# Performance work log

Hardware: AMD Instinct MI355X
Metric: run time of the kernel (lower is better)

## Reference

```python
import jax, jax.numpy as jnp
import numpy as np

TOKEN_SELF_ATTN_VALUE = -50000.0
EPS_NORM = 1e-12
EPS_SCATTER = 1e-5
COMMITMENT = 1e-4


def _l2norm(x):
    return x / jnp.maximum(jnp.linalg.norm(x, axis=-1, keepdims=True), EPS_NORM)


def _shift(x):
    # relative-position shift, faithful to the torch `shift` helper
    # x: [..., i, j] -> [..., i, j]
    *pre, i, j = x.shape
    x = jnp.concatenate([x, jnp.zeros((*pre, i, i), x.dtype)], axis=-1)  # [..., i, i+j]
    l = i + j - 1
    x = x.reshape(*pre, i * (i + j))
    pad = (-x.shape[-1]) % l
    x = jnp.concatenate([x, jnp.zeros((*pre, pad), x.dtype)], axis=-1)
    x = x.reshape(*pre, -1, l)
    return x[..., :i, i - 1:]


def setup_inputs() -> dict:
    key = jax.random.key(0)
    k1, k2, k3, k4 = jax.random.split(key, 4)
    b, h, t, d = 4, 8, 8192, 64
    c, wsz = 64, 128
    qk = jax.random.normal(k1, (b, h, t, d), jnp.float32)
    v = jax.random.normal(k2, (b, h, t, d), jnp.float32)
    means = jax.random.normal(k3, (h, c, d), jnp.float32)
    means = _l2norm(means)  # trained kmeans means are unit-normalized
    rel_w = jax.random.normal(k4, (wsz, h, d), jnp.float32) * 0.02
    return {"qk": qk, "v": v, "means": means, "rel_w": rel_w}


def reference(qk, v, means, rel_w):
    b, h, t, d = qk.shape
    c = means.shape[1]
    wsz = min(rel_w.shape[0], t)

    # ---- kmeans routing (eval path: no iterations, fixed means) ----
    k_routing = _l2norm(qk)                                   # [b,h,t,d]
    dists = jnp.einsum('bhld,hcd->bhlc', k_routing, means)    # cosine sims
    buckets = jnp.argmax(dists, axis=-1)                      # [b,h,t]
    # top-wsz tokens per cluster, sorted ascending (matches topk -> sort -> transpose)
    _, idx = jax.lax.top_k(jnp.swapaxes(dists, -1, -2), wsz)  # [b,h,c,wsz]
    indices = jnp.sort(idx, axis=-1).reshape(b, h, c * wsz)   # [b,h,c*wsz]

    # commitment loss against routed means (means is a non-trainable buffer)
    routed_means = means[jnp.arange(h)[None, :, None], buckets]  # [b,h,t,d]
    loss = jnp.mean((k_routing - routed_means) ** 2) * COMMITMENT

    # ---- gather routed windows ----
    qk_g = jnp.take_along_axis(qk, indices[..., None], axis=2).reshape(b, h, c, wsz, d)
    v_g = jnp.take_along_axis(v, indices[..., None], axis=2).reshape(b, h, c, wsz, d)
    q = qk_g
    k = _l2norm(qk_g)

    scale = d ** -0.5
    dots = jnp.einsum('bhnid,bhnjd->bhnij', q, k) * scale     # [b,h,c,wsz,wsz]
    rel = jnp.einsum('bhnid,jhd->bhnij', q, rel_w) * scale
    dots = dots + _shift(rel)

    # token cannot attend to itself within its window
    eye = jnp.eye(wsz, dtype=bool)
    dots = jnp.where(eye, TOKEN_SELF_ATTN_VALUE, dots)

    attn = jax.nn.softmax(dots, axis=-1)
    bo = jnp.einsum('bhnij,bhnjd->bhnid', attn, v_g).reshape(b, h, c * wsz, d)

    # ---- scatter-mean back to original token positions ----
    def scat(idx1, src1):  # idx1: [N], src1: [N,d]
        num = jnp.zeros((t, d), src1.dtype).at[idx1].add(src1)
        den = jnp.zeros((t, d), src1.dtype).at[idx1].add(jnp.ones_like(src1))
        return num / (den + EPS_SCATTER)

    out = jax.vmap(jax.vmap(scat))(indices, bo)               # [b,h,t,d]
    return out, loss
```

## Files before the change

kernel.cpp:

```cpp
#include <hip/hip_runtime.h>
#include <hip/hip_bf16.h>
#include <math.h>

#define NB 4
#define NH 8
#define TT 8192
#define DD 64
#define NC 64
#define WW 128
#define BHN 32
#define SCALE 0.125f
#define INVCAP 24
#define DTPB 64

typedef __bf16  bf16x8 __attribute__((ext_vector_type(8)));
typedef __bf16  bf16x4 __attribute__((ext_vector_type(4)));
typedef float   f32x4  __attribute__((ext_vector_type(4)));
typedef unsigned long long u64;
typedef unsigned int u32;

#define MFMA(a, b, c) __builtin_amdgcn_mfma_f32_16x16x32_bf16((a), (b), (c), 0, 0, 0)

__device__ __forceinline__ u32 fixkey32(float dv) {
    double k = ((double)dv + 1.0) * 2147483648.0;
    k = fmin(fmax(k, 0.0), 4294967295.0);
    return (u32)k;
}

#define QD_ADDR(row, gi) (((row) << 6) + ((((gi) ^ ((row) & 7))) << 3))

__global__ __launch_bounds__(256) void k_dists(
    const float* __restrict__ qk, const float* __restrict__ means,
    const float* __restrict__ rel_w, __bf16* __restrict__ relb,
    u32* __restrict__ keys, double* __restrict__ lossa)
{
    __shared__ __attribute__((aligned(16))) __bf16 qh[64 * 64], qm[64 * 64], ql[64 * 64];
    __shared__ __attribute__((aligned(16))) __bf16 ah[64 * 64], am[64 * 64], al[64 * 64];
    __shared__ float invS[DTPB], s2S[DTPB], mn2S[NC];
    __shared__ double red[4];

    const int bh = blockIdx.x, h = bh & 7, tid = threadIdx.x;
    const int t0 = blockIdx.y * DTPB;

    if (blockIdx.y == 0) {
        const float4* rw = (const float4*)rel_w;
#pragma unroll
        for (int k = 0; k < 2; k++) {
            const int i = bh * 512 + k * 256 + tid;
            const float4 v = rw[i];
            bf16x4 o;
            o[0] = (__bf16)v.x; o[1] = (__bf16)v.y; o[2] = (__bf16)v.z; o[3] = (__bf16)v.w;
            *(bf16x4*)(relb + i * 4) = o;
        }
    }

    {
        const int r = tid >> 2, qt = tid & 3;
        const float4* src = (const float4*)(means + (size_t)(h * NC + r) * DD + qt * 16);
        float4 f[4];
        f[0] = src[0]; f[1] = src[1]; f[2] = src[2]; f[3] = src[3];
        bf16x8 vh[2], vm[2], vl[2];
        float ssq = 0.f;
#pragma unroll
        for (int j = 0; j < 16; j++) {
            const float xx = ((const float*)f)[j];
            ssq = fmaf(xx, xx, ssq);
            const __bf16 hh_ = (__bf16)xx;
            const float r1 = xx - (float)hh_;
            const __bf16 mm_ = (__bf16)r1;
            const float r2 = r1 - (float)mm_;
            vh[j >> 3][j & 7] = hh_; vm[j >> 3][j & 7] = mm_; vl[j >> 3][j & 7] = (__bf16)r2;
        }
#pragma unroll
        for (int gg = 0; gg < 2; gg++) {
            const int dst = QD_ADDR(r, qt * 2 + gg);
            *(bf16x8*)(ah + dst) = vh[gg];
            *(bf16x8*)(am + dst) = vm[gg];
            *(bf16x8*)(al + dst) = vl[gg];
        }
        ssq += __shfl_xor(ssq, 1);
        ssq += __shfl_xor(ssq, 2);
        if (qt == 0) mn2S[r] = ssq;
    }
    {
        const int r = tid >> 2, qt = tid & 3;
        const float4* src = (const float4*)(qk + ((size_t)bh * TT + t0 + r) * DD + qt * 16);
        float4 f[4];
        f[0] = src[0]; f[1] = src[1]; f[2] = src[2]; f[3] = src[3];
        bf16x8 vh[2], vm[2], vl[2];
        float ssq = 0.f;
#pragma unroll
        for (int j = 0; j < 16; j++) {
            const float xx = ((const float*)f)[j];
            ssq = fmaf(xx, xx, ssq);
            const __bf16 hh_ = (__bf16)xx;
            const float r1 = xx - (float)hh_;
            const __bf16 mm_ = (__bf16)r1;
            const float r2 = r1 - (float)mm_;
            vh[j >> 3][j & 7] = hh_; vm[j >> 3][j & 7] = mm_; vl[j >> 3][j & 7] = (__bf16)r2;
        }
#pragma unroll
        for (int gg = 0; gg < 2; gg++) {
            const int dst = QD_ADDR(r, qt * 2 + gg);
            *(bf16x8*)(qh + dst) = vh[gg];
            *(bf16x8*)(qm + dst) = vm[gg];
            *(bf16x8*)(ql + dst) = vl[gg];
        }
        ssq += __shfl_xor(ssq, 1);
        ssq += __shfl_xor(ssq, 2);
        if (qt == 0) {
            const float inv = 1.0f / fmaxf(sqrtf(ssq), 1e-12f);
            invS[r] = inv;
            s2S[r] = ssq * inv * inv;
        }
    }
    __syncthreads();

    const int lane = tid & 63, wv = tid >> 6;
    const int lo = lane & 15, quad = lane >> 4;

    bf16x8 Bh[2], Bm[2], Bl[2];
    {
        const int row = wv * 16 + lo;
#pragma unroll
        for (int kh = 0; kh < 2; kh++) {
            const int src = QD_ADDR(row, kh * 4 + quad);
            Bh[kh] = *(const bf16x8*)(qh + src);
            Bm[kh] = *(const bf16x8*)(qm + src);
            Bl[kh] = *(const bf16x8*)(ql + src);
        }
    }

    f32x4 acc[4];
#pragma unroll
    for (int ct = 0; ct < 4; ct++) {
        bf16x8 Ah[2], Am[2], Al[2];
#pragma unroll
        for (int kh = 0; kh < 2; kh++) {
            const int src = QD_ADDR(ct * 16 + lo, kh * 4 + quad);
            Ah[kh] = *(const bf16x8*)(ah + src);
            Am[kh] = *(const bf16x8*)(am + src);
            Al[kh] = *(const bf16x8*)(al + src);
        }
        f32x4 a = (f32x4){0.f, 0.f, 0.f, 0.f};
        a = MFMA(Al[0], Bm[0], a); a = MFMA(Al[1], Bm[1], a);
        a = MFMA(Am[0], Bl[0], a); a = MFMA(Am[1], Bl[1], a);
        a = MFMA(Am[0], Bm[0], a); a = MFMA(Am[1], Bm[1], a);
        a = MFMA(Ah[0], Bl[0], a); a = MFMA(Ah[1], Bl[1], a);
        a = MFMA(Al[0], Bh[0], a); a = MFMA(Al[1], Bh[1], a);
        a = MFMA(Am[0], Bh[0], a); a = MFMA(Am[1], Bh[1], a);
        a = MFMA(Ah[0], Bm[0], a); a = MFMA(Ah[1], Bm[1], a);
        a = MFMA(Ah[0], Bh[0], a); a = MFMA(Ah[1], Bh[1], a);
        acc[ct] = a;
    }

    const int tok = wv * 16 + lo;
    const float inv = invS[tok];
    float rawmax = -3.0e38f; int cbest = 0;
    u32* kout = keys + (size_t)bh * NC * TT + (size_t)(t0 + tok);
#pragma unroll
    for (int ct = 0; ct < 4; ct++)
#pragma unroll
        for (int r = 0; r < 4; r++) {
            const float raw = acc[ct][r];
            const int c = ct * 16 + quad * 4 + r;
            if (raw > rawmax) { rawmax = raw; cbest = c; }
            kout[(size_t)c * TT] = fixkey32(raw * inv);
        }

#pragma unroll
    for (int off = 16; off < 64; off <<= 1) {
        const float ov = __shfl_xor(rawmax, off);
        const int   oc = __shfl_xor(cbest, off);
        if (ov > rawmax || (ov == rawmax && oc < cbest)) { rawmax = ov; cbest = oc; }
    }
    double lt_lane = 0.0;
    if (quad == 0)
        lt_lane = (double)(s2S[tok] + mn2S[cbest] - 2.0f * rawmax * inv);

#pragma unroll
    for (int o = 32; o; o >>= 1) lt_lane += __shfl_xor(lt_lane, o);
    if (lane == 0) red[wv] = lt_lane;
    __syncthreads();
    if (tid == 0) atomicAdd(lossa, red[0] + red[1] + red[2] + red[3]);
}

__global__ __launch_bounds__(256) void k_topk(
    const u32* __restrict__ keys, int* __restrict__ indices,
    unsigned int* __restrict__ cnt, unsigned short* __restrict__ inv)
{
    __shared__ unsigned int hist[4][256];
    __shared__ int wsum[8];
    __shared__ int bc_bin, bc_rank, bc_cnt;

    const int bhc = blockIdx.x, tid = threadIdx.x;
    const int wv = tid >> 6, lane = tid & 63;
    const int bh = bhc >> 6;

    u32 key[32];
    {
        const uint4* p = (const uint4*)(keys + (size_t)bhc * TT + tid * 32);
#pragma unroll
        for (int i = 0; i < 8; i++) {
            uint4 u = p[i];
            key[4*i] = u.x; key[4*i+1] = u.y; key[4*i+2] = u.z; key[4*i+3] = u.w;
        }
    }

    u32 thr = 0;
    int need = 128, gshift = 24, prevShift = 0;
    unsigned int* hb = &hist[0][0];

    for (int level = 0; level < 4; level++) {
        const int shift = 24 - 8 * level;
        hb[tid] = 0; hb[tid + 256] = 0; hb[tid + 512] = 0; hb[tid + 768] = 0;
        __syncthreads();
        unsigned int* hw = hist[wv];
        if (level == 0) {
#pragma unroll
            for (int i = 0; i < 32; i++)
                atomicAdd(&hw[key[i] >> 24], 1u);
        } else {
            const u32 pv = thr >> prevShift;
#pragma unroll
            for (int i = 0; i < 32; i++)
                if ((key[i] >> prevShift) == pv)
                    atomicAdd(&hw[(key[i] >> shift) & 255u], 1u);
        }
        __syncthreads();

        const int b = 255 - tid;
        const int c = hist[0][b] + hist[1][b] + hist[2][b] + hist[3][b];
        int incl = c;
#pragma unroll
        for (int o = 1; o < 64; o <<= 1) {
            const int v = __shfl_up(incl, o);
            if (lane >= o) incl += v;
        }
        if (lane == 63) wsum[wv] = incl;
        __syncthreads();
        int above = incl - c;
        for (int wj = 0; wj < wv; wj++) above += wsum[wj];
        if (above < need && above + c >= need) {
            bc_bin = b; bc_rank = above; bc_cnt = c;
        }
        __syncthreads();
        thr |= ((u32)bc_bin) << shift;
        need -= bc_rank;
        gshift = shift;
        prevShift = shift;
        if (bc_cnt == need || shift == 0) break;
    }

    const u32 tg = thr >> gshift;
    int cgt = 0, ceq = 0;
#pragma unroll
    for (int i = 0; i < 32; i++) {
        const u32 kg = key[i] >> gshift;
        cgt += (kg > tg) ? 1 : 0;
        ceq += (kg == tg) ? 1 : 0;
    }
    int ig = cgt, ie = ceq;
#pragma unroll
    for (int o = 1; o < 64; o <<= 1) {
        const int vg = __shfl_up(ig, o);
        const int ve = __shfl_up(ie, o);
        if (lane >= o) { ig += vg; ie += ve; }
    }
    if (lane == 63) { wsum[wv] = ig; wsum[4 + wv] = ie; }
    __syncthreads();
    int pgt = ig - cgt, peq = ie - ceq;
    for (int wj = 0; wj < wv; wj++) { pgt += wsum[wj]; peq += wsum[4 + wj]; }

    const int rneed = need;
    int* outp = indices + bhc * WW;
    unsigned int* cntb = cnt + (bh << 13);
    unsigned short* invb = inv + (((size_t)bh << 13) * INVCAP);
    const int cbase = (bhc & 63) * WW;
    int g = 0, e = 0;
#pragma unroll
    for (int i = 0; i < 32; i++) {
        const int tok = tid * 32 + i;
        const u32 kg = key[i] >> gshift;
        if (kg > tg) {
            const int tb = (peq + e < rneed) ? (peq + e) : rneed;
            const int wpos = pgt + g + tb;
            outp[wpos] = tok;
            const unsigned int pos = atomicAdd(&cntb[tok], 1u);
            if (pos < INVCAP) invb[(size_t)tok * INVCAP + pos] = (unsigned short)(cbase + wpos);
            g++;
        } else if (kg == tg) {
            if (peq + e < rneed) {
                const int wpos = pgt + g + peq + e;
                outp[wpos] = tok;
                const unsigned int pos = atomicAdd(&cntb[tok], 1u);
                if (pos < INVCAP) invb[(size_t)tok * INVCAP + pos] = (unsigned short)(cbase + wpos);
            }
            e++;
        }
    }
}

#define QS_ADDR(row, gi) (((row) << 6) + ((((gi) ^ ((row) & 7))) << 3))

__global__ __launch_bounds__(512) void k_attn(
    const float* __restrict__ qk, const float* __restrict__ vin,
    const __bf16* __restrict__ relb, const int* __restrict__ indices,
    float* __restrict__ bo)
{
    __shared__ __attribute__((aligned(16))) __bf16 uv[64 * 136];
    __shared__ __attribute__((aligned(16))) __bf16 rs[128 * 136];
    __shared__ float invs[128];

    const int tid  = threadIdx.x;
    const int lane = tid & 63;
    const int wv   = tid >> 6;
    const int lo   = lane & 15;
    const int quad = lane >> 4;
    const int rbase = wv * 16;

    const int bhc = blockIdx.x;
    const int bh  = bhc >> 6;
    const int h   = bh & 7;

    const int r  = tid >> 2;
    const int qp = tid & 3;
    const int rowidx = indices[bhc * WW + r];
    const size_t rowoff = ((size_t)bh * TT + rowidx) * DD + qp * 16;
    float4 q0, q1, q2, q3, vreg[4];
    {
        const float4* qsrc = (const float4*)(qk + rowoff);
        q0 = qsrc[0]; q1 = qsrc[1]; q2 = qsrc[2]; q3 = qsrc[3];
        const float4* vsrc = (const float4*)(vin + rowoff);
        vreg[0] = vsrc[0]; vreg[1] = vsrc[1]; vreg[2] = vsrc[2]; vreg[3] = vsrc[3];
    }
    {
        float ssq = q0.x*q0.x + q0.y*q0.y + q0.z*q0.z + q0.w*q0.w
                  + q1.x*q1.x + q1.y*q1.y + q1.z*q1.z + q1.w*q1.w
                  + q2.x*q2.x + q2.y*q2.y + q2.z*q2.z + q2.w*q2.w
                  + q3.x*q3.x + q3.y*q3.y + q3.z*q3.z + q3.w*q3.w;
        ssq += __shfl_xor(ssq, 1);
        ssq += __shfl_xor(ssq, 2);
        if (qp == 0) invs[r] = 1.0f / fmaxf(sqrtf(ssq), 1e-12f);
        bf16x8 va, vb;
        va[0]=(__bf16)q0.x; va[1]=(__bf16)q0.y; va[2]=(__bf16)q0.z; va[3]=(__bf16)q0.w;
        va[4]=(__bf16)q1.x; va[5]=(__bf16)q1.y; va[6]=(__bf16)q1.z; va[7]=(__bf16)q1.w;
        vb[0]=(__bf16)q2.x; vb[1]=(__bf16)q2.y; vb[2]=(__bf16)q2.z; vb[3]=(__bf16)q2.w;
        vb[4]=(__bf16)q3.x; vb[5]=(__bf16)q3.y; vb[6]=(__bf16)q3.z; vb[7]=(__bf16)q3.w;
        *(bf16x8*)(uv + QS_ADDR(r, qp * 2))     = va;
        *(bf16x8*)(uv + QS_ADDR(r, qp * 2 + 1)) = vb;
    }
    __syncthreads();

    f32x4 acc[8];

#pragma unroll
    for (int nt = 0; nt < 8; nt++) acc[nt] = (f32x4){0.f, 0.f, 0.f, 0.f};
#pragma unroll
    for (int k0 = 0; k0 < 64; k0 += 32) {
        bf16x8 qa = *(const bf16x8*)(uv + QS_ADDR(rbase + lo, (k0 >> 3) + quad));
#pragma unroll
        for (int nt = 0; nt < 8; nt++) {
            const bf16x8 wb = *(const bf16x8*)(relb + ((nt * 16 + lo) * 8 + h) * 64 + k0 + quad * 8);
            acc[nt] = MFMA(qa, wb, acc[nt]);
        }
    }
#pragma unroll
    for (int nt = 0; nt < 8; nt++)
#pragma unroll
        for (int rg = 0; rg < 4; rg++)
            rs[(rbase + quad * 4 + rg) * 136 + nt * 16 + lo] = (__bf16)acc[nt][rg];

#pragma unroll
    for (int nt = 0; nt < 8; nt++) acc[nt] = (f32x4){0.f, 0.f, 0.f, 0.f};
#pragma unroll
    for (int k0 = 0; k0 < 64; k0 += 32) {
        bf16x8 qa = *(const bf16x8*)(uv + QS_ADDR(rbase + lo, (k0 >> 3) + quad));
#pragma unroll
        for (int nt = 0; nt < 8; nt++) {
            bf16x8 qb = *(const bf16x8*)(uv + QS_ADDR(nt * 16 + lo, (k0 >> 3) + quad));
            acc[nt] = MFMA(qa, qb, acc[nt]);
        }
    }

    float inv_j[8];
#pragma unroll
    for (int nt = 0; nt < 8; nt++) inv_j[nt] = invs[nt * 16 + lo];

#pragma unroll
    for (int rg = 0; rg < 4; rg++) {
        const int i = rbase + quad * 4 + rg;
#pragma unroll
        for (int nt = 0; nt < 8; nt++) {
            const int j = nt * 16 + lo;
            float val = acc[nt][rg] * inv_j[nt] * SCALE;
            if (j <= i) val += SCALE * (float)rs[i * 136 + (j + 127 - i)];
            if (j == i) val = -50000.0f;
            acc[nt][rg] = val;
        }
    }

#pragma unroll
    for (int rg = 0; rg < 4; rg++) {
        float m = -3.0e38f;
#pragma unroll
        for (int nt = 0; nt < 8; nt++) m = fmaxf(m, acc[nt][rg]);
#pragma unroll
        for (int msk = 1; msk < 16; msk <<= 1) m = fmaxf(m, __shfl_xor(m, msk));
        float s = 0.f;
#pragma unroll
        for (int nt = 0; nt < 8; nt++) {
            const float e = __expf(acc[nt][rg] - m);
            acc[nt][rg] = e; s += e;
        }
#pragma unroll
        for (int msk = 1; msk < 16; msk <<= 1) s += __shfl_xor(s, msk);
        const float is = 1.0f / s;
        const int i = rbase + quad * 4 + rg;
#pragma unroll
        for (int nt = 0; nt < 8; nt++)
            rs[i * 136 + nt * 16 + lo] = (__bf16)(acc[nt][rg] * is);
    }
    __syncthreads();

    __bf16* vt = uv;
#pragma unroll
    for (int i = 0; i < 4; i++) {
        vt[(qp * 16 + 4*i + 0) * 136 + r] = (__bf16)vreg[i].x;
        vt[(qp * 16 + 4*i + 1) * 136 + r] = (__bf16)vreg[i].y;
        vt[(qp * 16 + 4*i + 2) * 136 + r] = (__bf16)vreg[i].z;
        vt[(qp * 16 + 4*i + 3) * 136 + r] = (__bf16)vreg[i].w;
    }
    __syncthreads();

    f32x4 accO[4];
#pragma unroll
    for (int nt = 0; nt < 4; nt++) accO[nt] = (f32x4){0.f, 0.f, 0.f, 0.f};
#pragma unroll
    for (int k0 = 0; k0 < 128; k0 += 32) {
        bf16x8 pa = *(const bf16x8*)(rs + (rbase + lo) * 136 + k0 + quad * 8);
#pragma unroll
        for (int nt = 0; nt < 4; nt++) {
            bf16x8 vb = *(const bf16x8*)(vt + (nt * 16 + lo) * 136 + k0 + quad * 8);
            accO[nt] = MFMA(pa, vb, accO[nt]);
        }
    }

    float* bb = bo + (size_t)bhc * (WW * DD);
#pragma unroll
    for (int rg = 0; rg < 4; rg++) {
        const int i = rbase + quad * 4 + rg;
#pragma unroll
        for (int nt = 0; nt < 4; nt++)
            bb[(size_t)i * DD + nt * 16 + lo] = accO[nt][rg];
    }
}

__global__ __launch_bounds__(256) void k_out(
    const float* __restrict__ bo, const unsigned int* __restrict__ cnt,
    const unsigned short* __restrict__ inv, const double* __restrict__ lossa,
    float* __restrict__ out)
{
    const int tid = threadIdx.x;
    const int g = blockIdx.x * 16 + (tid >> 4);
    const int l = tid & 15;
    const int bh = g >> 13;
    const unsigned int n = cnt[g];
    const int nc = (n < (unsigned)INVCAP) ? (int)n : INVCAP;
    const unsigned short* ip = inv + (size_t)g * INVCAP;
    const float* bbase = bo + (((size_t)bh << 13) * DD) + l * 4;

    const uint4 ipv = *(const uint4*)ip;
    const int s0 = ipv.x & 0xffff, s1 = ipv.x >> 16;
    const int s2 = ipv.y & 0xffff, s3 = ipv.y >> 16;
    const int s4 = ipv.z & 0xffff, s5 = ipv.z >> 16;
    const int s6 = ipv.w & 0xffff, s7 = ipv.w >> 16;

    float4 a0 = {0.f,0.f,0.f,0.f}, a1 = a0, a2 = a0, a3 = a0;
    float4 a4 = a0, a5 = a0, a6 = a0, a7 = a0;
    if (nc > 0) a0 = *(const float4*)(bbase + (size_t)s0 * DD);
    if (nc > 1) a1 = *(const float4*)(bbase + (size_t)s1 * DD);
    if (nc > 2) a2 = *(const float4*)(bbase + (size_t)s2 * DD);
    if (nc > 3) a3 = *(const float4*)(bbase + (size_t)s3 * DD);
    if (nc > 4) a4 = *(const float4*)(bbase + (size_t)s4 * DD);
    if (nc > 5) a5 = *(const float4*)(bbase + (size_t)s5 * DD);
    if (nc > 6) a6 = *(const float4*)(bbase + (size_t)s6 * DD);
    if (nc > 7) a7 = *(const float4*)(bbase + (size_t)s7 * DD);

    float4 s;
    s.x = ((a0.x + a1.x) + (a2.x + a3.x)) + ((a4.x + a5.x) + (a6.x + a7.x));
    s.y = ((a0.y + a1.y) + (a2.y + a3.y)) + ((a4.y + a5.y) + (a6.y + a7.y));
    s.z = ((a0.z + a1.z) + (a2.z + a3.z)) + ((a4.z + a5.z) + (a6.z + a7.z));
    s.w = ((a0.w + a1.w) + (a2.w + a3.w)) + ((a4.w + a5.w) + (a6.w + a7.w));

    for (int e = 8; e < nc; e++) {
        const int slot = ip[e];
        const float4 v4 = *(const float4*)(bbase + (size_t)slot * DD);
        s.x += v4.x; s.y += v4.y; s.z += v4.z; s.w += v4.w;
    }

    const float r = 1.0f / ((float)n + 1e-5f);
    s.x *= r; s.y *= r; s.z *= r; s.w *= r;
    *(float4*)(out + (size_t)g * DD + l * 4) = s;
    if (g == 0 && l == 0) out[16777216] = (float)(lossa[0] * (0.0001 / 16777216.0));
}

extern "C" void kernel_launch(void* const* d_in, const int* in_sizes, int n_in,
                              void* d_out, int out_size, void* d_ws, size_t ws_size,
                              hipStream_t stream) {
    (void)in_sizes; (void)n_in; (void)ws_size; (void)out_size;
    const float* qk    = (const float*)d_in[0];
    const float* v     = (const float*)d_in[1];
    const float* means = (const float*)d_in[2];
    const float* rel_w = (const float*)d_in[3];
    float* out = (float*)d_out;

    char* ws = (char*)d_ws;
    const size_t KEYS_B = (size_t)BHN * NC * TT * 4;
    const size_t IDX_B  = (size_t)BHN * NC * WW * 4;
    const size_t CNT_B  = (size_t)BHN * TT * 4;
    const size_t INV_B  = (size_t)BHN * TT * INVCAP * 2;
    u32*            keys  = (u32*)ws;
    float*          bo    = (float*)ws;
    int*            idx   = (int*)(ws + KEYS_B);
    unsigned int*   cnt   = (unsigned int*)(ws + KEYS_B + IDX_B);
    double*         lossa = (double*)(ws + KEYS_B + IDX_B + CNT_B);
    unsigned short* inv   = (unsigned short*)(ws + KEYS_B + IDX_B + CNT_B + 4096);
    __bf16*         relb  = (__bf16*)(ws + KEYS_B + IDX_B + CNT_B + 4096 + INV_B);

    hipMemsetAsync(ws + KEYS_B + IDX_B, 0, CNT_B + 4096, stream);

    k_dists<<<dim3(BHN, TT / DTPB), 256, 0, stream>>>(qk, means, rel_w, relb, keys, lossa);
    k_topk<<<BHN * NC, 256, 0, stream>>>(keys, idx, cnt, inv);
    k_attn<<<BHN * NC, 512, 0, stream>>>(qk, v, relb, idx, bo);
    k_out<<<BHN * TT / 16, 256, 0, stream>>>(bo, cnt, inv, lossa, out);
}
```

Measured before the change: 326.2 us.

## Process four clusters per attention block with register prefetch of next tile

Each k_attn block now loops over four consecutive clusters instead of one, and the grid shrinks to match. While the current tile computes, the gathered q and v rows for the next tile are loaded into registers, so global gather latency overlaps with the MFMA and softmax work. The cost is fewer blocks (512 instead of 2048), which reduces parallelism across CUs. It also adds an extra barrier per tile and raises register pressure.

```diff
diff --git a/kernel.cpp b/kernel.cpp
--- a/kernel.cpp
+++ b/kernel.cpp
@@ -12,6 +12,7 @@
 #define SCALE 0.125f
 #define INVCAP 24
 #define DTPB 64
+#define NTILE 4
 
 typedef __bf16  bf16x8 __attribute__((ext_vector_type(8)));
 typedef __bf16  bf16x4 __attribute__((ext_vector_type(4)));
@@ -319,140 +320,168 @@
     const int quad = lane >> 4;
     const int rbase = wv * 16;
 
-    const int bhc = blockIdx.x;
-    const int bh  = bhc >> 6;
-    const int h   = bh & 7;
+    const int bhc0 = blockIdx.x * NTILE;
+    const int bh   = bhc0 >> 6;
+    const int h    = bh & 7;
 
     const int r  = tid >> 2;
     const int qp = tid & 3;
-    const int rowidx = indices[bhc * WW + r];
-    const size_t rowoff = ((size_t)bh * TT + rowidx) * DD + qp * 16;
-    float4 q0, q1, q2, q3, vreg[4];
+
+    float4 q0, q1, q2, q3, v0, v1, v2, v3;
     {
-        const float4* qsrc = (const float4*)(qk + rowoff);
+        const int idx0 = indices[bhc0 * WW + r];
+        const size_t ro = ((size_t)bh * TT + idx0) * DD + qp * 16;
+        const float4* qsrc = (const float4*)(qk + ro);
         q0 = qsrc[0]; q1 = qsrc[1]; q2 = qsrc[2]; q3 = qsrc[3];
-        const float4* vsrc = (const float4*)(vin + rowoff);
-        vreg[0] = vsrc[0]; vreg[1] = vsrc[1]; vreg[2] = vsrc[2]; vreg[3] = vsrc[3];
-    }
-    {
-        float ssq = q0.x*q0.x + q0.y*q0.y + q0.z*q0.z + q0.w*q0.w
-                  + q1.x*q1.x + q1.y*q1.y + q1.z*q1.z + q1.w*q1.w
-                  + q2.x*q2.x + q2.y*q2.y + q2.z*q2.z + q2.w*q2.w
-                  + q3.x*q3.x + q3.y*q3.y + q3.z*q3.z + q3.w*q3.w;
-        ssq += __shfl_xor(ssq, 1);
-        ssq += __shfl_xor(ssq, 2);
-        if (qp == 0) invs[r] = 1.0f / fmaxf(sqrtf(ssq), 1e-12f);
-        bf16x8 va, vb;
-        va[0]=(__bf16)q0.x; va[1]=(__bf16)q0.y; va[2]=(__bf16)q0.z; va[3]=(__bf16)q0.w;
-        va[4]=(__bf16)q1.x; va[5]=(__bf16)q1.y; va[6]=(__bf16)q1.z; va[7]=(__bf16)q1.w;
-        vb[0]=(__bf16)q2.x; vb[1]=(__bf16)q2.y; vb[2]=(__bf16)q2.z; vb[3]=(__bf16)q2.w;
-        vb[4]=(__bf16)q3.x; vb[5]=(__bf16)q3.y; vb[6]=(__bf16)q3.z; vb[7]=(__bf16)q3.w;
-        *(bf16x8*)(uv + QS_ADDR(r, qp * 2))     = va;
-        *(bf16x8*)(uv + QS_ADDR(r, qp * 2 + 1)) = vb;
-    }
-    __syncthreads();
-
-    f32x4 acc[8];
-
-#pragma unroll
-    for (int nt = 0; nt < 8; nt++) acc[nt] = (f32x4){0.f, 0.f, 0.f, 0.f};
-#pragma unroll
-    for (int k0 = 0; k0 < 64; k0 += 32) {
-        bf16x8 qa = *(const bf16x8*)(uv + QS_ADDR(rbase + lo, (k0 >> 3) + quad));
-#pragma unroll
-        for (int nt = 0; nt < 8; nt++) {
-            const bf16x8 wb = *(const bf16x8*)(relb + ((nt * 16 + lo) * 8 + h) * 64 + k0 + quad * 8);
-            acc[nt] = MFMA(qa, wb, acc[nt]);
-        }
-    }
-#pragma unroll
-    for (int nt = 0; nt < 8; nt++)
-#pragma unroll
-        for (int rg = 0; rg < 4; rg++)
-            rs[(rbase + quad * 4 + rg) * 136 + nt * 16 + lo] = (__bf16)acc[nt][rg];
-
-#pragma unroll
-    for (int nt = 0; nt < 8; nt++) acc[nt] = (f32x4){0.f, 0.f, 0.f, 0.f};
-#pragma unroll
-    for (int k0 = 0; k0 < 64; k0 += 32) {
-        bf16x8 qa = *(const bf16x8*)(uv + QS_ADDR(rbase + lo, (k0 >> 3) + quad));
-#pragma unroll
-        for (int nt = 0; nt < 8; nt++) {
-            bf16x8 qb = *(const bf16x8*)(uv + QS_ADDR(nt * 16 + lo, (k0 >> 3) + quad));
-            acc[nt] = MFMA(qa, qb, acc[nt]);
-        }
-    }
-
-    float inv_j[8];
-#pragma unroll
-    for (int nt = 0; nt < 8; nt++) inv_j[nt] = invs[nt * 16 + lo];
-
-#pragma unroll
-    for (int rg = 0; rg < 4; rg++) {
-        const int i = rbase + quad * 4 + rg;
-#pragma unroll
-        for (int nt = 0; nt < 8; nt++) {
-            const int j = nt * 16 + lo;
-            float val = acc[nt][rg] * inv_j[nt] * SCALE;
-            if (j <= i) val += SCALE * (float)rs[i * 136 + (j + 127 - i)];
-            if (j == i) val = -50000.0f;
-            acc[nt][rg] = val;
-        }
-    }
-
-#pragma unroll
-    for (int rg = 0; rg < 4; rg++) {
-        float m = -3.0e38f;
-#pragma unroll
-        for (int nt = 0; nt < 8; nt++) m = fmaxf(m, acc[nt][rg]);
-#pragma unroll
-        for (int msk = 1; msk < 16; msk <<= 1) m = fmaxf(m, __shfl_xor(m, msk));
-        float s = 0.f;
-#pragma unroll
-        for (int nt = 0; nt < 8; nt++) {
-            const float e = __expf(acc[nt][rg] - m);
-            acc[nt][rg] = e; s += e;
-        }
-#pragma unroll
-        for (int msk = 1; msk < 16; msk <<= 1) s += __shfl_xor(s, msk);
-        const float is = 1.0f / s;
-        const int i = rbase + quad * 4 + rg;
+        const float4* vsrc = (const float4*)(vin + ro);
+        v0 = vsrc[0]; v1 = vsrc[1]; v2 = vsrc[2]; v3 = vsrc[3];
+    }
+
+    for (int t = 0; t < NTILE; t++) {
+        const int bhc = bhc0 + t;
+
+        {
+            float ssq = q0.x*q0.x + q0.y*q0.y + q0.z*q0.z + q0.w*q0.w
+                      + q1.x*q1.x + q1.y*q1.y + q1.z*q1.z + q1.w*q1.w
+                      + q2.x*q2.x + q2.y*q2.y + q2.z*q2.z + q2.w*q2.w
+                      + q3.x*q3.x + q3.y*q3.y + q3.z*q3.z + q3.w*q3.w;
+            ssq += __shfl_xor(ssq, 1);
+            ssq += __shfl_xor(ssq, 2);
+            if (qp == 0) invs[r] = 1.0f / fmaxf(sqrtf(ssq), 1e-12f);
+            bf16x8 va, vb;
+            va[0]=(__bf16)q0.x; va[1]=(__bf16)q0.y; va[2]=(__bf16)q0.z; va[3]=(__bf16)q0.w;
+            va[4]=(__bf16)q1.x; va[5]=(__bf16)q1.y; va[6]=(__bf16)q1.z; va[7]=(__bf16)q1.w;
+            vb[0]=(__bf16)q2.x; vb[1]=(__bf16)q2.y; vb[2]=(__bf16)q2.z; vb[3]=(__bf16)q2.w;
+            vb[4]=(__bf16)q3.x; vb[5]=(__bf16)q3.y; vb[6]=(__bf16)q3.z; vb[7]=(__bf16)q3.w;
+            *(bf16x8*)(uv + QS_ADDR(r, qp * 2))     = va;
+            *(bf16x8*)(uv + QS_ADDR(r, qp * 2 + 1)) = vb;
+        }
+        __syncthreads();
+
+        int nidx = 0;
+        if (t + 1 < NTILE) {
+            nidx = indices[(bhc + 1) * WW + r];
+            const float4* qn = (const float4*)(qk + ((size_t)bh * TT + nidx) * DD + qp * 16);
+            q0 = qn[0]; q1 = qn[1]; q2 = qn[2]; q3 = qn[3];
+        }
+
+        f32x4 acc[8];
+
+#pragma unroll
+        for (int nt = 0; nt < 8; nt++) acc[nt] = (f32x4){0.f, 0.f, 0.f, 0.f};
+#pragma unroll
+        for (int k0 = 0; k0 < 64; k0 += 32) {
+            bf16x8 qa = *(const bf16x8*)(uv + QS_ADDR(rbase + lo, (k0 >> 3) + quad));
+#pragma unroll
+            for (int nt = 0; nt < 8; nt++) {
+                const bf16x8 wb = *(const bf16x8*)(relb + ((nt * 16 + lo) * 8 + h) * 64 + k0 + quad * 8);
+                acc[nt] = MFMA(qa, wb, acc[nt]);
+            }
+        }
 #pragma unroll
         for (int nt = 0; nt < 8; nt++)
-            rs[i * 136 + nt * 16 + lo] = (__bf16)(acc[nt][rg] * is);
-    }
-    __syncthreads();
-
-    __bf16* vt = uv;
-#pragma unroll
-    for (int i = 0; i < 4; i++) {
-        vt[(qp * 16 + 4*i + 0) * 136 + r] = (__bf16)vreg[i].x;
-        vt[(qp * 16 + 4*i + 1) * 136 + r] = (__bf16)vreg[i].y;
-        vt[(qp * 16 + 4*i + 2) * 136 + r] = (__bf16)vreg[i].z;
-        vt[(qp * 16 + 4*i + 3) * 136 + r] = (__bf16)vreg[i].w;
-    }
-    __syncthreads();
-
-    f32x4 accO[4];
-#pragma unroll
-    for (int nt = 0; nt < 4; nt++) accO[nt] = (f32x4){0.f, 0.f, 0.f, 0.f};
-#pragma unroll
-    for (int k0 = 0; k0 < 128; k0 += 32) {
-        bf16x8 pa = *(const bf16x8*)(rs + (rbase + lo) * 136 + k0 + quad * 8);
-#pragma unroll
-        for (int nt = 0; nt < 4; nt++) {
-            bf16x8 vb = *(const bf16x8*)(vt + (nt * 16 + lo) * 136 + k0 + quad * 8);
-            accO[nt] = MFMA(pa, vb, accO[nt]);
-        }
-    }
-
-    float* bb = bo + (size_t)bhc * (WW * DD);
-#pragma unroll
-    for (int rg = 0; rg < 4; rg++) {
-        const int i = rbase + quad * 4 + rg;
-#pragma unroll
-        for (int nt = 0; nt < 4; nt++)
-            bb[(size_t)i * DD + nt * 16 + lo] = accO[nt][rg];
+#pragma unroll
+            for (int rg = 0; rg < 4; rg++)
+                rs[(rbase + quad * 4 + rg) * 136 + nt * 16 + lo] = (__bf16)acc[nt][rg];
+
+#pragma unroll
+        for (int nt = 0; nt < 8; nt++) acc[nt] = (f32x4){0.f, 0.f, 0.f, 0.f};
+#pragma unroll
+        for (int k0 = 0; k0 < 64; k0 += 32) {
+            bf16x8 qa = *(const bf16x8*)(uv + QS_ADDR(rbase + lo, (k0 >> 3) + quad));
+#pragma unroll
+            for (int nt = 0; nt < 8; nt++) {
+                bf16x8 qb = *(const bf16x8*)(uv + QS_ADDR(nt * 16 + lo, (k0 >> 3) + quad));
+                acc[nt] = MFMA(qa, qb, acc[nt]);
+            }
+        }
+
+        float inv_j[8];
+#pragma unroll
+        for (int nt = 0; nt < 8; nt++) inv_j[nt] = invs[nt * 16 + lo];
+
+#pragma unroll
+        for (int rg = 0; rg < 4; rg++) {
+            const int i = rbase + quad * 4 + rg;
+#pragma unroll
+            for (int nt = 0; nt < 8; nt++) {
+                const int j = nt * 16 + lo;
+                float val = acc[nt][rg] * inv_j[nt] * SCALE;
+                if (j <= i) val += SCALE * (float)rs[i * 136 + (j + 127 - i)];
+                if (j == i) val = -50000.0f;
+                acc[nt][rg] = val;
+            }
+        }
+
+#pragma unroll
+        for (int rg = 0; rg < 4; rg++) {
+            float m = -3.0e38f;
+#pragma unroll
+            for (int nt = 0; nt < 8; nt++) m = fmaxf(m, acc[nt][rg]);
+#pragma unroll
+            for (int msk = 1; msk < 16; msk <<= 1) m = fmaxf(m, __shfl_xor(m, msk));
+            float s = 0.f;
+#pragma unroll
+            for (int nt = 0; nt < 8; nt++) {
+                const float e = __expf(acc[nt][rg] - m);
+                acc[nt][rg] = e; s += e;
+            }
+#pragma unroll
+            for (int msk = 1; msk < 16; msk <<= 1) s += __shfl_xor(s, msk);
+            const float is = 1.0f / s;
+            const int i = rbase + quad * 4 + rg;
+#pragma unroll
+            for (int nt = 0; nt < 8; nt++)
+                rs[i * 136 + nt * 16 + lo] = (__bf16)(acc[nt][rg] * is);
+        }
+        __syncthreads();
+
+        __bf16* vt = uv;
+        vt[(qp * 16 +  0) * 136 + r] = (__bf16)v0.x;
+        vt[(qp * 16 +  1) * 136 + r] = (__bf16)v0.y;
+        vt[(qp * 16 +  2) * 136 + r] = (__bf16)v0.z;
+        vt[(qp * 16 +  3) * 136 + r] = (__bf16)v0.w;
+        vt[(qp * 16 +  4) * 136 + r] = (__bf16)v1.x;
+        vt[(qp * 16 +  5) * 136 + r] = (__bf16)v1.y;
+        vt[(qp * 16 +  6) * 136 + r] = (__bf16)v1.z;
+        vt[(qp * 16 +  7) * 136 + r] = (__bf16)v1.w;
+        vt[(qp * 16 +  8) * 136 + r] = (__bf16)v2.x;
+        vt[(qp * 16 +  9) * 136 + r] = (__bf16)v2.y;
+        vt[(qp * 16 + 10) * 136 + r] = (__bf16)v2.z;
+        vt[(qp * 16 + 11) * 136 + r] = (__bf16)v2.w;
+        vt[(qp * 16 + 12) * 136 + r] = (__bf16)v3.x;
+        vt[(qp * 16 + 13) * 136 + r] = (__bf16)v3.y;
+        vt[(qp * 16 + 14) * 136 + r] = (__bf16)v3.z;
+        vt[(qp * 16 + 15) * 136 + r] = (__bf16)v3.w;
+
+        if (t + 1 < NTILE) {
+            const float4* vn = (const float4*)(vin + ((size_t)bh * TT + nidx) * DD + qp * 16);
+            v0 = vn[0]; v1 = vn[1]; v2 = vn[2]; v3 = vn[3];
+        }
+        __syncthreads();
+
+        f32x4 accO[4];
+#pragma unroll
+        for (int nt = 0; nt < 4; nt++) accO[nt] = (f32x4){0.f, 0.f, 0.f, 0.f};
+#pragma unroll
+        for (int k0 = 0; k0 < 128; k0 += 32) {
+            bf16x8 pa = *(const bf16x8*)(rs + (rbase + lo) * 136 + k0 + quad * 8);
+#pragma unroll
+            for (int nt = 0; nt < 4; nt++) {
+                bf16x8 vb = *(const bf16x8*)(vt + (nt * 16 + lo) * 136 + k0 + quad * 8);
+                accO[nt] = MFMA(pa, vb, accO[nt]);
+            }
+        }
+
+        float* bb = bo + (size_t)bhc * (WW * DD);
+#pragma unroll
+        for (int rg = 0; rg < 4; rg++) {
+            const int i = rbase + quad * 4 + rg;
+#pragma unroll
+            for (int nt = 0; nt < 4; nt++)
+                bb[(size_t)i * DD + nt * 16 + lo] = accO[nt][rg];
+        }
+        __syncthreads();
     }
 }
 
@@ -532,6 +561,6 @@
 
     k_dists<<<dim3(BHN, TT / DTPB), 256, 0, stream>>>(qk, means, rel_w, relb, keys, lossa);
     k_topk<<<BHN * NC, 256, 0, stream>>>(keys, idx, cnt, inv);
-    k_attn<<<BHN * NC, 512, 0, stream>>>(qk, v, relb, idx, bo);
+    k_attn<<<BHN * NC / NTILE, 512, 0, stream>>>(qk, v, relb, idx, bo);
     k_out<<<BHN * TT / 16, 256, 0, stream>>>(bo, cnt, inv, lossa, out);
 }
```

After: 324.9 us. About the same (-0.4%).
